# Optimization experiments

Measured on AMD Instinct MI355X. Metric: run time of the kernel, lower is better.

## Reference

```python
import jax, jax.numpy as jnp
import numpy as np

# CapsuleConv2d(128, 256, 3, in_length=16, out_length=16, stride=1, padding=1,
#               share_weight=True, routing_type='k_means' (dot), num_iterations=3, squash=True)
KH = KW = 3
SH = SW = 1
PH = PW = 1
DH = DW = 1
IN_LENGTH = 16
OUT_LENGTH = 16
NUM_ITERS = 3
EPS = 1e-12


def _extract_patches(x):
    # x: [B, C, H, W] -> [B, C, KH, KW, OH, OW] (torch.nn.functional.unfold layout)
    B, C, H, W = x.shape
    OH = (H + 2 * PH - DH * (KH - 1) - 1) // SH + 1
    OW = (W + 2 * PW - DW * (KW - 1) - 1) // SW + 1
    xp = jnp.pad(x, ((0, 0), (0, 0), (PH, PH), (PW, PW)))
    rows = []
    for i in range(KH):  # small fixed kernel loop
        cols = []
        for j in range(KW):
            cols.append(xp[:, :, i * DH: i * DH + (OH - 1) * SH + 1: SH,
                              j * DW: j * DW + (OW - 1) * SW + 1: SW])
        rows.append(jnp.stack(cols, axis=2))
    return jnp.stack(rows, axis=2)  # [B, C, KH, KW, OH, OW]


def _k_means_routing(u, num_iterations):
    # u: [B, OH, OW, N_in, O, L]; routing over N_in (axis -3), dot similarity
    v = u.mean(axis=-3, keepdims=True)  # [B, OH, OW, 1, O, L]
    for _ in range(num_iterations):
        vn = v / jnp.maximum(jnp.linalg.norm(v, axis=-1, keepdims=True), EPS)
        logits = jnp.sum(u * vn, axis=-1, keepdims=True)      # [B,OH,OW,N_in,O,1]
        probs = jax.nn.softmax(logits, axis=-3)
        v = jnp.sum(probs * u, axis=-3, keepdims=True)
    return jnp.squeeze(v, axis=-3)  # [B, OH, OW, O, L]


def _squash(s):
    norm = jnp.linalg.norm(s, axis=-1, keepdims=True)
    return s * (norm / (1.0 + norm * norm))  # = ||s||^2/(1+||s||^2) * s/||s||


def setup_inputs() -> dict:
    key = jax.random.key(0)
    k1, k2 = jax.random.split(key)
    x = jax.random.normal(k1, (2, 128, 32, 32), dtype=jnp.float32)
    # weight: [O=out_channels//out_length, L=out_length, M=in_length, KH, KW]
    fan = IN_LENGTH * KH * KW + OUT_LENGTH * KH * KW
    bound = float(np.sqrt(6.0 / fan))  # xavier_uniform-ish scale
    weight = jax.random.uniform(k2, (16, 16, 16, 3, 3), dtype=jnp.float32,
                                minval=-bound, maxval=bound)
    return {"x": x, "weight": weight}


def reference(x, weight):
    B = x.shape[0]
    O, L, M = weight.shape[0], weight.shape[1], weight.shape[2]
    patches = _extract_patches(x)                      # [B, C, KH, KW, OH, OW]
    OH, OW = patches.shape[-2], patches.shape[-1]
    G = x.shape[1] // M
    patches = patches.reshape(B, G, M, KH, KW, OH, OW)
    # priors[b,h,w,g,i,j,o,l] = sum_m patch[b,g,m,i,j,h,w] * weight[o,l,m,i,j]
    priors = jnp.einsum('bgmijhw,olmij->bhwgijol', patches, weight)
    priors = priors.reshape(B, OH, OW, G * KH * KW, O, L)
    v = _k_means_routing(priors, NUM_ITERS)            # [B, OH, OW, O, L]
    v = _squash(v)
    out = v.reshape(B, OH, OW, O * L).transpose(0, 3, 1, 2)  # [B, C_out, OH, OW]
    return out
```

## Files before the change

kernel.cpp:

```cpp
#include <hip/hip_runtime.h>


typedef float v2f __attribute__((ext_vector_type(2)));
typedef int   i4  __attribute__((ext_vector_type(4)));
typedef short bh8 __attribute__((ext_vector_type(8)));
typedef float f16v __attribute__((ext_vector_type(16)));

#define STR 34
#define WBF_ELEMS 73728

#define DPP_ADD(a, ctrl)                                                     \
  a += __int_as_float(__builtin_amdgcn_update_dpp(                           \
          0, __float_as_int(a), ctrl, 0xF, 0xF, true))

__device__ __forceinline__ float dpp_add16(float x) {
    float s = x;
    DPP_ADD(s, 0x128); DPP_ADD(s, 0x124); DPP_ADD(s, 0x122); DPP_ADD(s, 0x121);
    return s;
}

__device__ __forceinline__ float swz16_add(float x) {
    int y = __builtin_amdgcn_ds_swizzle(__float_as_int(x), 0x401F);
    return x + __int_as_float(y);
}

__device__ __forceinline__ float red32(float x) {
    return swz16_add(dpp_add16(x));
}

__device__ __forceinline__ float xor32_add(float x) {
    return x + __shfl_xor(x, 32, 64);
}

__device__ __forceinline__ float frcp(float x) {
    return __builtin_amdgcn_rcpf(x);
}

__device__ __forceinline__ v2f pkfma(v2f a, v2f b, v2f c) {
    return __builtin_elementwise_fma(a, b, c);
}

__global__ __launch_bounds__(256)
void prep2_kernel(const float* __restrict__ x, const float* __restrict__ W,
                  i4* __restrict__ xP, unsigned short* __restrict__ Wbf) {
    const int blk = blockIdx.x;
    const int tid = threadIdx.x;
    if (blk < 64) {
        __shared__ float xs[128 * 33];
        const int b = blk >> 5, h = blk & 31;
        const float* xb = x + b * (128 * 32 * 32) + h * 32;
        #pragma unroll
        for (int k = 0; k < 16; ++k) {
            int idx = k * 256 + tid;
            int c = idx >> 5, w = idx & 31;
            xs[c * 33 + w] = xb[c * 1024 + w];
        }
        __syncthreads();
        i4* xo = xP + (b * 32 + h) * 1024;
        #pragma unroll
        for (int it = 0; it < 4; ++it) {
            int slot = it * 256 + tid;
            int s  = slot & 1;
            int hf = (slot >> 1) & 1;
            int gl = (slot >> 2) & 7;
            int w  = slot >> 5;
            int c0 = gl * 16 + hf * 8;
            float f0 = xs[(c0 + 0) * 33 + w], f1 = xs[(c0 + 1) * 33 + w];
            float f2 = xs[(c0 + 2) * 33 + w], f3 = xs[(c0 + 3) * 33 + w];
            float f4 = xs[(c0 + 4) * 33 + w], f5 = xs[(c0 + 5) * 33 + w];
            float f6 = xs[(c0 + 6) * 33 + w], f7 = xs[(c0 + 7) * 33 + w];
            unsigned b0 = __float_as_uint(f0), b1 = __float_as_uint(f1);
            unsigned b2 = __float_as_uint(f2), b3 = __float_as_uint(f3);
            unsigned b4 = __float_as_uint(f4), b5 = __float_as_uint(f5);
            unsigned b6 = __float_as_uint(f6), b7 = __float_as_uint(f7);
            i4 pk;
            if (s == 0) {
                pk.x = (int)((b0 >> 16) | (b1 & 0xFFFF0000u));
                pk.y = (int)((b2 >> 16) | (b3 & 0xFFFF0000u));
                pk.z = (int)((b4 >> 16) | (b5 & 0xFFFF0000u));
                pk.w = (int)((b6 >> 16) | (b7 & 0xFFFF0000u));
            } else {
                unsigned l0 = __float_as_uint(f0 - __uint_as_float(b0 & 0xFFFF0000u));
                unsigned l1 = __float_as_uint(f1 - __uint_as_float(b1 & 0xFFFF0000u));
                unsigned l2 = __float_as_uint(f2 - __uint_as_float(b2 & 0xFFFF0000u));
                unsigned l3 = __float_as_uint(f3 - __uint_as_float(b3 & 0xFFFF0000u));
                unsigned l4 = __float_as_uint(f4 - __uint_as_float(b4 & 0xFFFF0000u));
                unsigned l5 = __float_as_uint(f5 - __uint_as_float(b5 & 0xFFFF0000u));
                unsigned l6 = __float_as_uint(f6 - __uint_as_float(b6 & 0xFFFF0000u));
                unsigned l7 = __float_as_uint(f7 - __uint_as_float(b7 & 0xFFFF0000u));
                pk.x = (int)((l0 >> 16) | (l1 & 0xFFFF0000u));
                pk.y = (int)((l2 >> 16) | (l3 & 0xFFFF0000u));
                pk.z = (int)((l4 >> 16) | (l5 & 0xFFFF0000u));
                pk.w = (int)((l6 >> 16) | (l7 & 0xFFFF0000u));
            }
            xo[slot] = pk;
        }
    } else {
        int idx = (blk - 64) * 256 + tid;
        int j  = idx & 7;
        int L  = (idx >> 3) & 63;
        int s  = (idx >> 9) & 1;
        int tt = (idx >> 10) & 7;
        int ij = idx >> 13;
        int k  = (L >> 5) * 8 + j;
        int t  = tt * 32 + (L & 31);
        float wv = W[(t * 16 + k) * 9 + ij];
        unsigned bits = __float_as_uint(wv);
        unsigned hib  = bits & 0xFFFF0000u;
        unsigned short val;
        if (s == 0) val = (unsigned short)(hib >> 16);
        else {
            float lo = wv - __uint_as_float(hib);
            val = (unsigned short)(__float_as_uint(lo) >> 16);
        }
        Wbf[idx] = val;
    }
}

#define CWR(REG, IJ)                                                         \
    uLds[wroff + STR * ((((REG) >> 2) * 72) + (((REG) & 3) * 9) + (IJ))] =   \
        acc[(REG)];

#define ONEIJ(IJ) {                                                          \
    const int di = (IJ) / 3, dj = (IJ) % 3;                                  \
    const int hh = h + di - 1;                                               \
    const bool hok = (unsigned)hh < 32u;                                     \
    const int hhc = hok ? hh : 0;                                            \
    const int ww = w0 + pl + dj - 1;                                         \
    const bool ok = hok && ((unsigned)ww < 32u);                             \
    const int wwc = ok ? ww : 0;                                             \
    const int slot = (((bb * 32 + hhc) * 32 + wwc) * 8 + gl) * 2 + half;     \
    i4 ah = xpi4[slot * 2];                                                  \
    i4 al = xpi4[slot * 2 + 1];                                              \
    i4 bh = bfr[((IJ) * 8 + tt) * 128 + lane];                               \
    i4 bl = bfr[((IJ) * 8 + tt) * 128 + 64 + lane];                          \
    const i4 z_ = {0, 0, 0, 0};                                              \
    ah = ok ? ah : z_;                                                       \
    al = ok ? al : z_;                                                       \
    bh8 aHi = __builtin_bit_cast(bh8, ah);                                   \
    bh8 aLo = __builtin_bit_cast(bh8, al);                                   \
    bh8 bHi = __builtin_bit_cast(bh8, bh);                                   \
    bh8 bLo = __builtin_bit_cast(bh8, bl);                                   \
    f16v acc = {0.f,0.f,0.f,0.f,0.f,0.f,0.f,0.f,                             \
                0.f,0.f,0.f,0.f,0.f,0.f,0.f,0.f};                            \
    acc = __builtin_amdgcn_mfma_f32_32x32x16_bf16(aHi, bLo, acc, 0, 0, 0);   \
    acc = __builtin_amdgcn_mfma_f32_32x32x16_bf16(aLo, bHi, acc, 0, 0, 0);   \
    acc = __builtin_amdgcn_mfma_f32_32x32x16_bf16(aHi, bHi, acc, 0, 0, 0);   \
    CWR(0, IJ)  CWR(1, IJ)  CWR(2, IJ)  CWR(3, IJ)                           \
    CWR(4, IJ)  CWR(5, IJ)  CWR(6, IJ)  CWR(7, IJ)                           \
    CWR(8, IJ)  CWR(9, IJ)  CWR(10, IJ) CWR(11, IJ)                          \
    CWR(12, IJ) CWR(13, IJ) CWR(14, IJ) CWR(15, IJ) }

#define LROWV(U0_, U1_, U2_, U3_, OFF)                                       \
  { const v2f* r2_ = (const v2f*)(rb + (OFF) * STR);                         \
    U0_ = r2_[0]; U1_ = r2_[1]; U2_ = r2_[2]; U3_ = r2_[3]; }

#define DOTV(UK0, UK1, UK2, UK3)                                             \
  ({ v2f d_ = UK0 * V0;                                                      \
     d_ = pkfma(UK1, V1, d_); d_ = pkfma(UK2, V2, d_);                       \
     d_ = pkfma(UK3, V3, d_); xor32_add(d_.x + d_.y); })

#define MEANJ(J)                                                             \
  { v2f s_ = (U0##J + U1##J) + U2##J;                                        \
    V##J.x = red32(s_.x) * (1.0f / 72.0f);                                   \
    V##J.y = red32(s_.y) * (1.0f / 72.0f); }

#define UPDJ(J)                                                              \
  { v2f pv_ = e0v * U0##J;                                                   \
    pv_ = pkfma(e1v, U1##J, pv_); pv_ = pkfma(e2v, U2##J, pv_);              \
    V##J.x = red32(pv_.x) * rs;                                              \
    V##J.y = red32(pv_.y) * rs; }

__global__ __launch_bounds__(512, 4)
void capsule_v16(const i4* __restrict__ xpi4, const i4* __restrict__ bfr,
                 float* __restrict__ out) {
    __shared__ float uLds[4 * 72 * STR];
    const int blk = blockIdx.x;
    const int tt  = blk & 7;
    const int q   = blk >> 3;
    const int bb  = q >> 8;
    const int r   = q & 255;
    const int h   = r >> 3;
    const int w0  = (r & 7) << 2;
    const int tid = threadIdx.x;

    {
        const int lane = tid & 63;
        const int wv   = tid >> 6;
        const int pl   = (lane & 31) >> 3;
        const int gl   = lane & 7;
        const int half = lane >> 5;
        const int tl   = lane & 31;
        const int wroff = tl + STR * 9 * 4 * half;

        if      (wv == 0) { ONEIJ(0) ONEIJ(8) }
        else if (wv == 1) { ONEIJ(1) }
        else if (wv == 2) { ONEIJ(2) }
        else if (wv == 3) { ONEIJ(3) }
        else if (wv == 4) { ONEIJ(4) }
        else if (wv == 5) { ONEIJ(5) }
        else if (wv == 6) { ONEIJ(6) }
        else              { ONEIJ(7) }
    }
    __syncthreads();

    const int p  = tid >> 7;
    const int o2 = (tid >> 6) & 1;
    const int jh = (tid >> 5) & 1;
    const int sc = tid & 31;
    const bool has3 = (sc < 8);
    const float* rb = uLds + (p * 72 + sc) * STR + o2 * 16 + jh * 8;

    v2f U00, U01, U02, U03;
    v2f U10, U11, U12, U13;
    v2f U20, U21, U22, U23;
    U20 = U21 = U22 = U23 = (v2f){0.0f, 0.0f};
    LROWV(U00, U01, U02, U03, 0)
    LROWV(U10, U11, U12, U13, 32)
    if (has3) LROWV(U20, U21, U22, U23, 64)

    v2f V0, V1, V2, V3;
    MEANJ(0) MEANJ(1) MEANJ(2) MEANJ(3)

    #pragma unroll 1
    for (int it = 0; it < 3; ++it) {
        v2f ssv = V0 * V0;
        ssv = pkfma(V1, V1, ssv); ssv = pkfma(V2, V2, ssv);
        ssv = pkfma(V3, V3, ssv);
        float ss = xor32_add(ssv.x + ssv.y);
        float inv = frcp(fmaxf(sqrtf(ss), 1e-12f));

        float E0 = __expf(DOTV(U00, U01, U02, U03) * inv);
        float E1 = __expf(DOTV(U10, U11, U12, U13) * inv);
        float E2 = has3 ? __expf(DOTV(U20, U21, U22, U23) * inv) : 0.0f;
        float ssum = red32((E0 + E1) + E2);
        float rs = frcp(ssum);

        v2f e0v = {E0, E0}, e1v = {E1, E1}, e2v = {E2, E2};
        UPDJ(0) UPDJ(1) UPDJ(2) UPDJ(3)
    }

    v2f ssv = V0 * V0;
    ssv = pkfma(V1, V1, ssv); ssv = pkfma(V2, V2, ssv);
    ssv = pkfma(V3, V3, ssv);
    float ss = xor32_add(ssv.x + ssv.y);
    float scale = sqrtf(ss) * frcp(1.0f + ss);

    v2f aa0 = (sc & 4) ? V2 : V0;
    v2f aa1 = (sc & 4) ? V3 : V1;
    v2f bb0 = (sc & 2) ? aa1 : aa0;
    float res = ((sc & 1) ? bb0.y : bb0.x) * scale;
    if (sc < 8) {
        int tg = tt * 32 + o2 * 16 + jh * 8 + sc;
        out[((bb * 256 + tg) * 32 + h) * 32 + w0 + p] = res;
    }
}

__global__ __launch_bounds__(256, 1)
void capsule_fb(const float* __restrict__ x, const float* __restrict__ Wraw,
                float* __restrict__ out) {
    __shared__ float patch[9 * 128];
    const int blk = blockIdx.x;
    const int b = blk >> 10, h = (blk >> 5) & 31, w = blk & 31;
    const int t = threadIdx.x;

    const float* xb = x + b * (128 * 32 * 32);
    for (int idx = t; idx < 1152; idx += 256) {
        int c = idx / 9, ij = idx - c * 9;
        int di = ij / 3, dj = ij - di * 3;
        int hh = h + di - 1, ww = w + dj - 1;
        float v = 0.0f;
        if ((unsigned)hh < 32u && (unsigned)ww < 32u)
            v = xb[(c * 32 + hh) * 32 + ww];
        patch[ij * 128 + c] = v;
    }
    __syncthreads();

    float u[72];
    #pragma unroll
    for (int ij = 0; ij < 9; ++ij) {
        float wr[16];
        #pragma unroll
        for (int m = 0; m < 16; ++m) wr[m] = Wraw[(t * 16 + m) * 9 + ij];
        #pragma unroll
        for (int g = 0; g < 8; ++g) {
            float acc = 0.0f;
            #pragma unroll
            for (int m = 0; m < 16; ++m)
                acc = fmaf(patch[ij * 128 + g * 16 + m], wr[m], acc);
            u[g * 9 + ij] = acc;
        }
    }

    float v = 0.0f;
    #pragma unroll
    for (int n = 0; n < 72; ++n) v += u[n];
    v *= (1.0f / 72.0f);
    #pragma unroll 1
    for (int it = 0; it < 3; ++it) {
        float sg = dpp_add16(v * v);
        float vn = v * frcp(fmaxf(sqrtf(sg), 1e-12f));
        float ssum = 0.0f, vacc = 0.0f;
        #pragma unroll
        for (int n = 0; n < 72; ++n) {
            float pp = dpp_add16(u[n] * vn);
            float e = __expf(pp);
            ssum += e;
            vacc = fmaf(e, u[n], vacc);
        }
        v = vacc * frcp(ssum);
    }
    float sg = dpp_add16(v * v);
    float res = v * sqrtf(sg) * frcp(1.0f + sg);
    out[((b * 256 + t) * 32 + h) * 32 + w] = res;
}

extern "C" void kernel_launch(void* const* d_in, const int* in_sizes, int n_in,
                              void* d_out, int out_size, void* d_ws, size_t ws_size,
                              hipStream_t stream) {
    const float* x = (const float*)d_in[0];
    const float* W = (const float*)d_in[1];
    float* out = (float*)d_out;
    i4* xP = (i4*)d_ws;
    unsigned short* Wbf = (unsigned short*)((char*)d_ws + 1048576);

    const size_t need = 1048576 + (size_t)WBF_ELEMS * 2;
    if (ws_size >= need) {
        prep2_kernel<<<352, 256, 0, stream>>>(x, W, xP, Wbf);
        capsule_v16<<<4096, 512, 0, stream>>>(xP, (const i4*)Wbf, out);
    } else {
        capsule_fb<<<2048, 256, 0, stream>>>(x, W, out);
    }
}
```

Baseline: 89.97 us.

## Store priors as fp16 in LDS and shrink blocks to two waves

Capsule priors from the MFMA stage are now stored in shared memory as fp16 instead of fp32, halving LDS footprint and read traffic. The block shrinks from 512 to 128 threads: two waves each compute four or five of the nine kernel positions, and during routing each wave handles two pixels with 16-lane reductions (DPP/swizzle only) instead of 32-lane reductions using cross-half shuffles. This trades the MFMA work parallelism within a block and fp32 precision of stored priors for lower LDS use, cheaper reductions and more work per thread.

```diff
diff --git a/kernel.cpp b/kernel.cpp
--- a/kernel.cpp
+++ b/kernel.cpp
@@ -5,8 +5,9 @@
 typedef int   i4  __attribute__((ext_vector_type(4)));
 typedef short bh8 __attribute__((ext_vector_type(8)));
 typedef float f16v __attribute__((ext_vector_type(16)));
-
-#define STR 34
+typedef _Float16 h2v __attribute__((ext_vector_type(2)));
+
+#define STRH 34
 #define WBF_ELEMS 73728
 
 #define DPP_ADD(a, ctrl)                                                     \
@@ -24,20 +25,17 @@
     return x + __int_as_float(y);
 }
 
-__device__ __forceinline__ float red32(float x) {
-    return swz16_add(dpp_add16(x));
-}
-
-__device__ __forceinline__ float xor32_add(float x) {
-    return x + __shfl_xor(x, 32, 64);
-}
-
 __device__ __forceinline__ float frcp(float x) {
     return __builtin_amdgcn_rcpf(x);
 }
 
 __device__ __forceinline__ v2f pkfma(v2f a, v2f b, v2f c) {
     return __builtin_elementwise_fma(a, b, c);
+}
+
+__device__ __forceinline__ v2f i2f(int u) {
+    h2v h = __builtin_bit_cast(h2v, u);
+    return (v2f){(float)h.x, (float)h.y};
 }
 
 __global__ __launch_bounds__(256)
@@ -117,9 +115,9 @@
     }
 }
 
-#define CWR(REG, IJ)                                                         \
-    uLds[wroff + STR * ((((REG) >> 2) * 72) + (((REG) & 3) * 9) + (IJ))] =   \
-        acc[(REG)];
+#define CWRH(REG, IJ)                                                        \
+    uH[wroff + STRH * ((((REG) >> 2) * 72) + (((REG) & 3) * 9) + (IJ))] =    \
+        (_Float16)acc[(REG)];
 
 #define ONEIJ(IJ) {                                                          \
     const int di = (IJ) / 3, dj = (IJ) % 3;                                  \
@@ -146,35 +144,41 @@
     acc = __builtin_amdgcn_mfma_f32_32x32x16_bf16(aHi, bLo, acc, 0, 0, 0);   \
     acc = __builtin_amdgcn_mfma_f32_32x32x16_bf16(aLo, bHi, acc, 0, 0, 0);   \
     acc = __builtin_amdgcn_mfma_f32_32x32x16_bf16(aHi, bHi, acc, 0, 0, 0);   \
-    CWR(0, IJ)  CWR(1, IJ)  CWR(2, IJ)  CWR(3, IJ)                           \
-    CWR(4, IJ)  CWR(5, IJ)  CWR(6, IJ)  CWR(7, IJ)                           \
-    CWR(8, IJ)  CWR(9, IJ)  CWR(10, IJ) CWR(11, IJ)                          \
-    CWR(12, IJ) CWR(13, IJ) CWR(14, IJ) CWR(15, IJ) }
-
-#define LROWV(U0_, U1_, U2_, U3_, OFF)                                       \
-  { const v2f* r2_ = (const v2f*)(rb + (OFF) * STR);                         \
-    U0_ = r2_[0]; U1_ = r2_[1]; U2_ = r2_[2]; U3_ = r2_[3]; }
-
-#define DOTV(UK0, UK1, UK2, UK3)                                             \
-  ({ v2f d_ = UK0 * V0;                                                      \
-     d_ = pkfma(UK1, V1, d_); d_ = pkfma(UK2, V2, d_);                       \
-     d_ = pkfma(UK3, V3, d_); xor32_add(d_.x + d_.y); })
-
-#define MEANJ(J)                                                             \
-  { v2f s_ = (U0##J + U1##J) + U2##J;                                        \
-    V##J.x = red32(s_.x) * (1.0f / 72.0f);                                   \
-    V##J.y = red32(s_.y) * (1.0f / 72.0f); }
-
-#define UPDJ(J)                                                              \
-  { v2f pv_ = e0v * U0##J;                                                   \
-    pv_ = pkfma(e1v, U1##J, pv_); pv_ = pkfma(e2v, U2##J, pv_);              \
-    V##J.x = red32(pv_.x) * rs;                                              \
-    V##J.y = red32(pv_.y) * rs; }
-
-__global__ __launch_bounds__(512, 4)
-void capsule_v16(const i4* __restrict__ xpi4, const i4* __restrict__ bfr,
+    CWRH(0, IJ)  CWRH(1, IJ)  CWRH(2, IJ)  CWRH(3, IJ)                       \
+    CWRH(4, IJ)  CWRH(5, IJ)  CWRH(6, IJ)  CWRH(7, IJ)                       \
+    CWRH(8, IJ)  CWRH(9, IJ)  CWRH(10, IJ) CWRH(11, IJ)                      \
+    CWRH(12, IJ) CWRH(13, IJ) CWRH(14, IJ) CWRH(15, IJ) }
+
+#define LROWP(P, K) {                                                        \
+    const int* r_ = (const int*)(rb##P + (K) * 16 * STRH);                   \
+    U##K##P.x = r_[0]; U##K##P.y = r_[1]; U##K##P.z = r_[2]; U##K##P.w = r_[3]; }
+
+#define DOTP(P, K)                                                           \
+  ({ v2f d_ = i2f(U##K##P.x) * V0##P;                                        \
+     d_ = pkfma(i2f(U##K##P.y), V1##P, d_);                                  \
+     d_ = pkfma(i2f(U##K##P.z), V2##P, d_);                                  \
+     d_ = pkfma(i2f(U##K##P.w), V3##P, d_);                                  \
+     swz16_add(d_.x + d_.y); })
+
+#define MEANC(P, C, J) {                                                     \
+    v2f s_ = (i2f(U0##P.C) + i2f(U1##P.C)) + (i2f(U2##P.C) + i2f(U3##P.C))   \
+             + i2f(U4##P.C);                                                 \
+    V##J##P.x = dpp_add16(s_.x) * (1.0f / 72.0f);                            \
+    V##J##P.y = dpp_add16(s_.y) * (1.0f / 72.0f); }
+
+#define UPDC(P, C, J) {                                                      \
+    v2f pv_ = e0##P * i2f(U0##P.C);                                          \
+    pv_ = pkfma(e1##P, i2f(U1##P.C), pv_);                                   \
+    pv_ = pkfma(e2##P, i2f(U2##P.C), pv_);                                   \
+    pv_ = pkfma(e3##P, i2f(U3##P.C), pv_);                                   \
+    pv_ = pkfma(e4##P, i2f(U4##P.C), pv_);                                   \
+    V##J##P.x = dpp_add16(pv_.x) * rs##P;                                    \
+    V##J##P.y = dpp_add16(pv_.y) * rs##P; }
+
+__global__ __launch_bounds__(128, 4)
+void capsule_v17(const i4* __restrict__ xpi4, const i4* __restrict__ bfr,
                  float* __restrict__ out) {
-    __shared__ float uLds[4 * 72 * STR];
+    __shared__ _Float16 uH[4 * 72 * STRH];
     const int blk = blockIdx.x;
     const int tt  = blk & 7;
     const int q   = blk >> 3;
@@ -183,76 +187,104 @@
     const int h   = r >> 3;
     const int w0  = (r & 7) << 2;
     const int tid = threadIdx.x;
+    const int lane = tid & 63;
+    const int wv   = tid >> 6;
 
     {
-        const int lane = tid & 63;
-        const int wv   = tid >> 6;
         const int pl   = (lane & 31) >> 3;
         const int gl   = lane & 7;
         const int half = lane >> 5;
         const int tl   = lane & 31;
-        const int wroff = tl + STR * 9 * 4 * half;
-
-        if      (wv == 0) { ONEIJ(0) ONEIJ(8) }
-        else if (wv == 1) { ONEIJ(1) }
-        else if (wv == 2) { ONEIJ(2) }
-        else if (wv == 3) { ONEIJ(3) }
-        else if (wv == 4) { ONEIJ(4) }
-        else if (wv == 5) { ONEIJ(5) }
-        else if (wv == 6) { ONEIJ(6) }
-        else              { ONEIJ(7) }
+        const int wroff = tl + STRH * 9 * 4 * half;
+
+        if (wv == 0) { ONEIJ(0) ONEIJ(2) ONEIJ(4) ONEIJ(6) ONEIJ(8) }
+        else         { ONEIJ(1) ONEIJ(3) ONEIJ(5) ONEIJ(7) }
     }
     __syncthreads();
 
-    const int p  = tid >> 7;
-    const int o2 = (tid >> 6) & 1;
-    const int jh = (tid >> 5) & 1;
-    const int sc = tid & 31;
-    const bool has3 = (sc < 8);
-    const float* rb = uLds + (p * 72 + sc) * STR + o2 * 16 + jh * 8;
-
-    v2f U00, U01, U02, U03;
-    v2f U10, U11, U12, U13;
-    v2f U20, U21, U22, U23;
-    U20 = U21 = U22 = U23 = (v2f){0.0f, 0.0f};
-    LROWV(U00, U01, U02, U03, 0)
-    LROWV(U10, U11, U12, U13, 32)
-    if (has3) LROWV(U20, U21, U22, U23, 64)
-
-    v2f V0, V1, V2, V3;
-    MEANJ(0) MEANJ(1) MEANJ(2) MEANJ(3)
+    const int pA = 2 * wv, pB = 2 * wv + 1;
+    const int i6 = lane;
+    const int o2 = i6 >> 5;
+    const int jh = (i6 >> 4) & 1;
+    const int sc = i6 & 15;
+    const bool has5 = (sc < 8);
+    const _Float16* rbA = uH + (pA * 72 + sc) * STRH + o2 * 16 + jh * 8;
+    const _Float16* rbB = uH + (pB * 72 + sc) * STRH + o2 * 16 + jh * 8;
+
+    i4 U0A, U1A, U2A, U3A, U4A;
+    i4 U0B, U1B, U2B, U3B, U4B;
+    U4A = (i4){0,0,0,0}; U4B = (i4){0,0,0,0};
+    LROWP(A, 0) LROWP(B, 0)
+    LROWP(A, 1) LROWP(B, 1)
+    LROWP(A, 2) LROWP(B, 2)
+    LROWP(A, 3) LROWP(B, 3)
+    if (has5) { LROWP(A, 4) LROWP(B, 4) }
+
+    v2f V0A, V1A, V2A, V3A;
+    v2f V0B, V1B, V2B, V3B;
+    MEANC(A, x, 0) MEANC(A, y, 1) MEANC(A, z, 2) MEANC(A, w, 3)
+    MEANC(B, x, 0) MEANC(B, y, 1) MEANC(B, z, 2) MEANC(B, w, 3)
 
     #pragma unroll 1
     for (int it = 0; it < 3; ++it) {
-        v2f ssv = V0 * V0;
-        ssv = pkfma(V1, V1, ssv); ssv = pkfma(V2, V2, ssv);
-        ssv = pkfma(V3, V3, ssv);
-        float ss = xor32_add(ssv.x + ssv.y);
-        float inv = frcp(fmaxf(sqrtf(ss), 1e-12f));
-
-        float E0 = __expf(DOTV(U00, U01, U02, U03) * inv);
-        float E1 = __expf(DOTV(U10, U11, U12, U13) * inv);
-        float E2 = has3 ? __expf(DOTV(U20, U21, U22, U23) * inv) : 0.0f;
-        float ssum = red32((E0 + E1) + E2);
-        float rs = frcp(ssum);
-
-        v2f e0v = {E0, E0}, e1v = {E1, E1}, e2v = {E2, E2};
-        UPDJ(0) UPDJ(1) UPDJ(2) UPDJ(3)
-    }
-
-    v2f ssv = V0 * V0;
-    ssv = pkfma(V1, V1, ssv); ssv = pkfma(V2, V2, ssv);
-    ssv = pkfma(V3, V3, ssv);
-    float ss = xor32_add(ssv.x + ssv.y);
-    float scale = sqrtf(ss) * frcp(1.0f + ss);
-
-    v2f aa0 = (sc & 4) ? V2 : V0;
-    v2f aa1 = (sc & 4) ? V3 : V1;
-    v2f bb0 = (sc & 2) ? aa1 : aa0;
-    float res = ((sc & 1) ? bb0.y : bb0.x) * scale;
+        v2f svA = V0A * V0A;
+        svA = pkfma(V1A, V1A, svA); svA = pkfma(V2A, V2A, svA);
+        svA = pkfma(V3A, V3A, svA);
+        float ssA = swz16_add(svA.x + svA.y);
+        v2f svB = V0B * V0B;
+        svB = pkfma(V1B, V1B, svB); svB = pkfma(V2B, V2B, svB);
+        svB = pkfma(V3B, V3B, svB);
+        float ssB = swz16_add(svB.x + svB.y);
+        float invA = frcp(fmaxf(sqrtf(ssA), 1e-12f));
+        float invB = frcp(fmaxf(sqrtf(ssB), 1e-12f));
+
+        float E0A = __expf(DOTP(A, 0) * invA);
+        float E0B = __expf(DOTP(B, 0) * invB);
+        float E1A = __expf(DOTP(A, 1) * invA);
+        float E1B = __expf(DOTP(B, 1) * invB);
+        float E2A = __expf(DOTP(A, 2) * invA);
+        float E2B = __expf(DOTP(B, 2) * invB);
+        float E3A = __expf(DOTP(A, 3) * invA);
+        float E3B = __expf(DOTP(B, 3) * invB);
+        float E4A = has5 ? __expf(DOTP(A, 4) * invA) : 0.0f;
+        float E4B = has5 ? __expf(DOTP(B, 4) * invB) : 0.0f;
+        float ssumA = dpp_add16(((E0A + E1A) + (E2A + E3A)) + E4A);
+        float ssumB = dpp_add16(((E0B + E1B) + (E2B + E3B)) + E4B);
+        float rsA = frcp(ssumA);
+        float rsB = frcp(ssumB);
+
+        v2f e0A = {E0A, E0A}, e1A = {E1A, E1A}, e2A = {E2A, E2A};
+        v2f e3A = {E3A, E3A}, e4A = {E4A, E4A};
+        v2f e0B = {E0B, E0B}, e1B = {E1B, E1B}, e2B = {E2B, E2B};
+        v2f e3B = {E3B, E3B}, e4B = {E4B, E4B};
+        UPDC(A, x, 0) UPDC(A, y, 1) UPDC(A, z, 2) UPDC(A, w, 3)
+        UPDC(B, x, 0) UPDC(B, y, 1) UPDC(B, z, 2) UPDC(B, w, 3)
+    }
+
+    v2f svA = V0A * V0A;
+    svA = pkfma(V1A, V1A, svA); svA = pkfma(V2A, V2A, svA);
+    svA = pkfma(V3A, V3A, svA);
+    float ssA = swz16_add(svA.x + svA.y);
+    float scaleA = sqrtf(ssA) * frcp(1.0f + ssA);
+    v2f svB = V0B * V0B;
+    svB = pkfma(V1B, V1B, svB); svB = pkfma(V2B, V2B, svB);
+    svB = pkfma(V3B, V3B, svB);
+    float ssB = swz16_add(svB.x + svB.y);
+    float scaleB = sqrtf(ssB) * frcp(1.0f + ssB);
+
     if (sc < 8) {
-        int tg = tt * 32 + o2 * 16 + jh * 8 + sc;
-        out[((bb * 256 + tg) * 32 + h) * 32 + w0 + p] = res;
+        const int tg = tt * 32 + o2 * 16 + jh * 8 + sc;
+        v2f a0A = (sc & 4) ? V2A : V0A;
+        v2f a1A = (sc & 4) ? V3A : V1A;
+        v2f b0A = (sc & 2) ? a1A : a0A;
+        float resA = ((sc & 1) ? b0A.y : b0A.x) * scaleA;
+        out[((bb * 256 + tg) * 32 + h) * 32 + w0 + pA] = resA;
+
+        v2f a0B = (sc & 4) ? V2B : V0B;
+        v2f a1B = (sc & 4) ? V3B : V1B;
+        v2f b0B = (sc & 2) ? a1B : a0B;
+        float resB = ((sc & 1) ? b0B.y : b0B.x) * scaleB;
+        out[((bb * 256 + tg) * 32 + h) * 32 + w0 + pB] = resB;
     }
 }
 
@@ -327,7 +359,7 @@
     const size_t need = 1048576 + (size_t)WBF_ELEMS * 2;
     if (ws_size >= need) {
         prep2_kernel<<<352, 256, 0, stream>>>(x, W, xP, Wbf);
-        capsule_v16<<<4096, 512, 0, stream>>>(xP, (const i4*)Wbf, out);
+        capsule_v17<<<4096, 128, 0, stream>>>(xP, (const i4*)Wbf, out);
     } else {
         capsule_fb<<<2048, 256, 0, stream>>>(x, W, out);
     }
```

Measured after the change: 83.08 us. 7.7% less time.
